# Kernel tuning notes

Hardware: AMD Instinct MI355X
Metric: run time of the kernel (lower is better)

Reference implementation:

```python
import jax, jax.numpy as jnp
import numpy as np

N = 100000   # num nodes
E = 600000   # num edges
H = 128      # hidden dim
R = 8        # num relations
B = 4        # num bases


def setup_inputs() -> dict:
    key = jax.random.key(0)
    ks = jax.random.split(key, 12)
    return {
        "node_ids": jnp.arange(N, dtype=jnp.int64 if jax.config.jax_enable_x64 else jnp.int32),
        "src": jax.random.randint(ks[0], (E,), 0, N),
        "dst": jax.random.randint(ks[1], (E,), 0, N),
        "etype": jax.random.randint(ks[2], (E,), 0, R),
        "embedding": jax.random.normal(ks[3], (N, H), dtype=jnp.float32),
        "V1": jax.random.normal(ks[4], (B, H, H), dtype=jnp.float32) * 0.05,
        "comp1": jax.random.normal(ks[5], (R, B), dtype=jnp.float32),
        "loop1": jax.random.normal(ks[6], (H, H), dtype=jnp.float32) * 0.05,
        "bias1": jax.random.normal(ks[7], (H,), dtype=jnp.float32) * 0.05,
        "V2": jax.random.normal(ks[8], (B, H, H), dtype=jnp.float32) * 0.05,
        "comp2": jax.random.normal(ks[9], (R, B), dtype=jnp.float32),
        "loop2": jax.random.normal(ks[10], (H, H), dtype=jnp.float32) * 0.05,
        "bias2": jax.random.normal(ks[11], (H,), dtype=jnp.float32) * 0.05,
    }


def _rgcn_layer(h, src, dst, etype, V, comp, loopW, bias, activate):
    # basis decomposition: W_r = sum_b comp[r,b] * V[b]   -> [R, in, out]
    W = jnp.einsum('rb,bio->rio', comp, V)
    # transform all nodes under all relations once (avoids per-edge GEMM): [N, R, out]
    hw = jnp.einsum('ni,rio->nro', h, W)
    # gather per-edge message for its (src, relation): [E, out]
    m = hw[src, etype]
    # scatter-sum aggregation at destination nodes
    agg = jax.ops.segment_sum(m, dst, num_segments=h.shape[0])
    out = agg + bias + h @ loopW  # bias + self-loop
    return jax.nn.relu(out) if activate else out


def reference(node_ids, src, dst, etype, embedding,
              V1, comp1, loop1, bias1,
              V2, comp2, loop2, bias2):
    h = embedding[node_ids]                       # EmbeddingLayer
    h = _rgcn_layer(h, src, dst, etype, V1, comp1, loop1, bias1, activate=True)
    h = _rgcn_layer(h, src, dst, etype, V2, comp2, loop2, bias2, activate=False)
    return h
```

## Files before the change

kernel.cpp:

```cpp
#include <hip/hip_runtime.h>
#include <hip/hip_bf16.h>

#define NN 100000
#define NE 600000
#define HH 128
#define NB 4
#define TILE 2048
#define NTILES ((NN + TILE - 1) / TILE)

typedef __attribute__((ext_vector_type(8))) short bf16x8;
typedef __attribute__((ext_vector_type(4))) float f32x4;
typedef __attribute__((ext_vector_type(4))) float vfloat4;
typedef __attribute__((ext_vector_type(4))) unsigned short ushort4v;

static __device__ __forceinline__ short f2bf(float f) {
  unsigned u = __float_as_uint(f);
  unsigned r = (u + 0x7fffu + ((u >> 16) & 1u)) >> 16;
  return (short)r;
}

static __device__ __forceinline__ void build_one(const float* __restrict__ V,
                                                 const float* __restrict__ loopW,
                                                 short* __restrict__ W8, int idx)
{
  int j  = idx & 7;
  int o  = (idx >> 3) & 127;
  int kb = idx >> 10;
  int k  = kb * 8 + j;
  float v;
  if (k < 512) v = V[(size_t)k * HH + o];
  else         v = loopW[(size_t)(k - 512) * HH + o];
  W8[idx] = f2bf(v);
}

__global__ __launch_bounds__(256) void prep_all(
    const float* __restrict__ V1, const float* __restrict__ loop1, short* __restrict__ W81,
    const float* __restrict__ V2, const float* __restrict__ loop2, short* __restrict__ W82,
    const float* __restrict__ emb, short* __restrict__ hbf1)
{
  const int bid = blockIdx.x;
  if (bid < 320) {
    build_one(V1, loop1, W81, bid * 256 + threadIdx.x);
  } else if (bid < 640) {
    build_one(V2, loop2, W82, (bid - 320) * 256 + threadIdx.x);
  } else {
    const int n8 = NN * HH / 8;
    int i = (bid - 640) * 256 + threadIdx.x;
    for (; i < n8; i += 800 * 256) {
      const vfloat4* p = reinterpret_cast<const vfloat4*>(emb + (size_t)i * 8);
      vfloat4 a = p[0], b = p[1];
      bf16x8 o;
#pragma unroll
      for (int j = 0; j < 4; ++j) { o[j] = f2bf(a[j]); o[j + 4] = f2bf(b[j]); }
      reinterpret_cast<bf16x8*>(hbf1)[i] = o;
    }
  }
}


__global__ __launch_bounds__(256) void hist_deg(const int* __restrict__ dst,
                                                int* __restrict__ deg)
{
  int e = blockIdx.x * blockDim.x + threadIdx.x;
  if (e < NE) atomicAdd(&deg[dst[e]], 1);
}

__global__ __launch_bounds__(256) void scan_tiles(const int* __restrict__ deg,
                                                  int* __restrict__ tilesum)
{
  __shared__ int red[256];
  const int tid = threadIdx.x;
  int base = blockIdx.x * TILE + tid * 8;
  int s = 0;
#pragma unroll
  for (int j = 0; j < 8; ++j) {
    int i = base + j;
    if (i < NN) s += deg[i];
  }
  red[tid] = s;
  __syncthreads();
  for (int off = 128; off > 0; off >>= 1) {
    if (tid < off) red[tid] += red[tid + off];
    __syncthreads();
  }
  if (tid == 0) tilesum[blockIdx.x] = red[0];
}

__global__ __launch_bounds__(256) void scan_final(const int* deg,
                                                  const int* __restrict__ tilesum,
                                                  int* __restrict__ rowptr,
                                                  int* cursor)
{
  __shared__ int lds[256];
  const int tid = threadIdx.x;
  int pre = 0;
  for (int t = 0; t < NTILES; ++t)
    if (t < blockIdx.x) pre += tilesum[t];

  int base = blockIdx.x * TILE + tid * 8;
  int d[8];
  int s = 0;
#pragma unroll
  for (int j = 0; j < 8; ++j) {
    int i = base + j;
    d[j] = (i < NN) ? deg[i] : 0;
    s += d[j];
  }
  lds[tid] = s;
  __syncthreads();
  for (int off = 1; off < 256; off <<= 1) {
    int t = (tid >= off) ? lds[tid - off] : 0;
    __syncthreads();
    lds[tid] += t;
    __syncthreads();
  }
  int run = pre + lds[tid] - s;
#pragma unroll
  for (int j = 0; j < 8; ++j) {
    int i = base + j;
    if (i < NN) {
      rowptr[i] = run;
      cursor[i] = run;
      run += d[j];
    }
  }
  if (blockIdx.x == NTILES - 1 && tid == 255)
    rowptr[NN] = pre + lds[255];
}

__global__ __launch_bounds__(256) void scatter_edges(
    const int* __restrict__ src, const int* __restrict__ dst, const int* __restrict__ ety,
    int* __restrict__ cursor, int* __restrict__ csr)
{
  int e = blockIdx.x * blockDim.x + threadIdx.x;
  if (e >= NE) return;
  int d = dst[e];
  int p = atomicAdd(&cursor[d], 1);
  csr[p] = src[e] | (ety[e] << 20);
}

template<int FINAL>
__global__ __launch_bounds__(512, 6) void rgcn_fused(
    const int* __restrict__ rowptr, const int* __restrict__ csr,
    const float* __restrict__ comp,
    const short* __restrict__ hbf,
    const short* __restrict__ W8,
    const float* __restrict__ bias,
    short* __restrict__ outH,
    float* __restrict__ outF)
{
  __shared__ bf16x8 gl[32][64];
  __shared__ bf16x8 wl[2][512];

  const int tid  = threadIdx.x;
  const int wave = tid >> 6;
  const int lane = tid & 63;
  const int b  = lane >> 4;
  const int q  = lane & 15;
  const int base = blockIdx.x * 32;
  const int l4 = lane * 4;

  const int mt = wave >> 2;
  const int ct0 = (wave & 3) * 2;
  const int mynode = base + mt * 16 + q;

  const bf16x8* wsrc = reinterpret_cast<const bf16x8*>(W8);
  bf16x8 w0reg = wsrc[tid];

  const char* hbytes = reinterpret_cast<const char*>(hbf);
  unsigned* glu = reinterpret_cast<unsigned*>(gl);

#pragma unroll 1
  for (int pp = 0; pp < 2; ++pp) {
    const int row0 = wave * 4 + pp * 2;
    const int row1 = row0 + 1;
    int       i0 = __builtin_amdgcn_readfirstlane(rowptr[base + row0]);
    const int E0 = __builtin_amdgcn_readfirstlane(rowptr[base + row0 + 1]);
    int       i1 = E0;
    const int E1 = __builtin_amdgcn_readfirstlane(rowptr[base + row1 + 1]);

    float a0[8] = {0.f, 0.f, 0.f, 0.f, 0.f, 0.f, 0.f, 0.f};
    float a1[8] = {0.f, 0.f, 0.f, 0.f, 0.f, 0.f, 0.f, 0.f};

    while (i0 < E0 || i1 < E1) {
      const bool d0 = i0 < E0, d1 = i1 < E1;
      unsigned hq[8];
      float    cq[8][4];
      if (d0) {
#pragma unroll
        for (int j = 0; j < 4; ++j) {
          const int idx = i0 + j;
          const bool v = idx < E0;
          const int e = __builtin_amdgcn_readfirstlane(csr[v ? idx : E0 - 1]);
          hq[j] = *reinterpret_cast<const unsigned*>(
              hbytes + (((size_t)(e & 0xFFFFF)) << 8) + l4);
#pragma unroll
          for (int B = 0; B < 4; ++B)
            cq[j][B] = v ? comp[(e >> 20) * NB + B] : 0.f;
        }
      }
      if (d1) {
#pragma unroll
        for (int j = 0; j < 4; ++j) {
          const int idx = i1 + j;
          const bool v = idx < E1;
          const int e = __builtin_amdgcn_readfirstlane(csr[v ? idx : E1 - 1]);
          hq[4 + j] = *reinterpret_cast<const unsigned*>(
              hbytes + (((size_t)(e & 0xFFFFF)) << 8) + l4);
#pragma unroll
          for (int B = 0; B < 4; ++B)
            cq[4 + j][B] = v ? comp[(e >> 20) * NB + B] : 0.f;
        }
      }
      if (d0) {
#pragma unroll
        for (int j = 0; j < 4; ++j) {
          const float lo = __uint_as_float(hq[j] << 16);
          const float hi = __uint_as_float(hq[j] & 0xffff0000u);
#pragma unroll
          for (int B = 0; B < 4; ++B) {
            a0[2 * B]     += cq[j][B] * lo;
            a0[2 * B + 1] += cq[j][B] * hi;
          }
        }
        i0 += 4;
      }
      if (d1) {
#pragma unroll
        for (int j = 0; j < 4; ++j) {
          const float lo = __uint_as_float(hq[4 + j] << 16);
          const float hi = __uint_as_float(hq[4 + j] & 0xffff0000u);
#pragma unroll
          for (int B = 0; B < 4; ++B) {
            a1[2 * B]     += cq[4 + j][B] * lo;
            a1[2 * B + 1] += cq[4 + j][B] * hi;
          }
        }
        i1 += 4;
      }
    }

#pragma unroll
    for (int B = 0; B < 4; ++B) {
      unsigned w0 = ((unsigned)(unsigned short)f2bf(a0[2 * B + 1]) << 16) |
                    (unsigned short)f2bf(a0[2 * B]);
      unsigned w1 = ((unsigned)(unsigned short)f2bf(a1[2 * B + 1]) << 16) |
                    (unsigned short)f2bf(a1[2 * B]);
      const int s = B * 16 + (lane >> 2);
      glu[row0 * 256 + ((s ^ (row0 & 7)) << 2) + (lane & 3)] = w0;
      glu[row1 * 256 + ((s ^ (row1 & 7)) << 2) + (lane & 3)] = w1;
    }
  }

  const bf16x8* ha = reinterpret_cast<const bf16x8*>(hbf + (size_t)mynode * HH);
  bf16x8 hreg[4];
#pragma unroll
  for (int j = 0; j < 4; ++j) hreg[j] = ha[j * 4 + b];

  wl[0][tid] = w0reg;
  __syncthreads();

  const int r  = q;
  const int g8 = b;

  f32x4 acc0 = {0.f, 0.f, 0.f, 0.f};
  f32x4 acc1 = {0.f, 0.f, 0.f, 0.f};

#pragma unroll 1
  for (int ks = 0; ks < 20; ++ks) {
    const int cur = ks & 1;
    bf16x8 nxt;
    if (ks < 19) nxt = wsrc[(ks + 1) * 512 + tid];
    bf16x8 a = (ks < 16) ? gl[mt * 16 + r][(ks * 4 + g8) ^ (r & 7)] : hreg[ks - 16];
    bf16x8 w0 = wl[cur][g8 * 128 + (ct0 + 0) * 16 + r];
    bf16x8 w1 = wl[cur][g8 * 128 + (ct0 + 1) * 16 + r];
    acc0 = __builtin_amdgcn_mfma_f32_16x16x32_bf16(w0, a, acc0, 0, 0, 0);
    acc1 = __builtin_amdgcn_mfma_f32_16x16x32_bf16(w1, a, acc1, 0, 0, 0);
    if (ks < 19) wl[cur ^ 1][tid] = nxt;
    __syncthreads();
  }

  if (FINAL) {
    float* glf = reinterpret_cast<float*>(gl);
#pragma unroll
    for (int c = 0; c < 2; ++c) {
      const f32x4 acc = c ? acc1 : acc0;
      const int row = mt * 16 + r;
      const int o = (ct0 + c) * 16 + g8 * 4;
      vfloat4 bs = *reinterpret_cast<const vfloat4*>(bias + o);
      vfloat4 x;
#pragma unroll
      for (int rr = 0; rr < 4; ++rr) x[rr] = acc[rr] + bs[rr];
      const int s = (ct0 + c) * 4 + g8;
      const int phys = s ^ (row & 7);
      *reinterpret_cast<vfloat4*>(glf + row * 128 + phys * 4) = x;
    }
    __syncthreads();
#pragma unroll
    for (int p = 0; p < 2; ++p) {
      const int flat = p * 512 + tid;
      const int row = flat >> 5, s = flat & 31;
      const int phys = s ^ (row & 7);
      vfloat4 x = *reinterpret_cast<const vfloat4*>(glf + row * 128 + phys * 4);
      *reinterpret_cast<vfloat4*>(outF + (size_t)(base + row) * HH + s * 4) = x;
    }
  } else {
    short* glb = reinterpret_cast<short*>(gl);
#pragma unroll
    for (int c = 0; c < 2; ++c) {
      const f32x4 acc = c ? acc1 : acc0;
      const int row = mt * 16 + r;
      const int o = (ct0 + c) * 16 + g8 * 4;
      vfloat4 bs = *reinterpret_cast<const vfloat4*>(bias + o);
      ushort4v sv;
#pragma unroll
      for (int rr = 0; rr < 4; ++rr)
        sv[rr] = (unsigned short)f2bf(fmaxf(acc[rr] + bs[rr], 0.f));
      const int u8 = (ct0 + c) * 4 + g8;
      const int phys16 = (u8 >> 1) ^ (row & 7);
      *reinterpret_cast<ushort4v*>(glb + row * 128 + phys16 * 8 + (u8 & 1) * 4) = sv;
    }
    __syncthreads();
    {
      const int row = tid >> 4, s16 = tid & 15;
      const int phys = s16 ^ (row & 7);
      bf16x8 x = *reinterpret_cast<const bf16x8*>(glb + row * 128 + phys * 8);
      *reinterpret_cast<bf16x8*>(outH + (size_t)(base + row) * HH + s16 * 8) = x;
    }
  }
}

extern "C" void kernel_launch(void* const* d_in, const int* in_sizes, int n_in,
                              void* d_out, int out_size, void* d_ws, size_t ws_size,
                              hipStream_t stream)
{
  const int*   srcp  = (const int*)d_in[1];
  const int*   dstp  = (const int*)d_in[2];
  const int*   etp   = (const int*)d_in[3];
  const float* emb   = (const float*)d_in[4];
  const float* V1    = (const float*)d_in[5];
  const float* comp1 = (const float*)d_in[6];
  const float* loop1 = (const float*)d_in[7];
  const float* bias1 = (const float*)d_in[8];
  const float* V2    = (const float*)d_in[9];
  const float* comp2 = (const float*)d_in[10];
  const float* loop2 = (const float*)d_in[11];
  const float* bias2 = (const float*)d_in[12];
  float* out = (float*)d_out;

  char* ws = (char*)d_ws;
  short* Wt1     = (short*)(ws);
  short* Wt2     = (short*)(ws + 163840);
  short* hbf1    = (short*)(ws + 327680);
  short* hbf2    = (short*)(ws + 25927680);
  int*   deg     = (int*)  (ws + 51527680);
  int*   rowptr  = (int*)  (ws + 51927680);
  int*   csr     = (int*)  (ws + 52327696);
  int*   tilesum = (int*)  (ws + 54727696);

  const int fused_blocks = NN / 32;
  const int e_blocks     = (NE + 255) / 256;

  hipMemsetAsync(deg, 0, NN * sizeof(int), stream);
  hipLaunchKernelGGL(hist_deg, dim3(e_blocks), dim3(256), 0, stream, dstp, deg);
  hipLaunchKernelGGL(scan_tiles, dim3(NTILES), dim3(256), 0, stream, deg, tilesum);
  hipLaunchKernelGGL(scan_final, dim3(NTILES), dim3(256), 0, stream,
                     deg, tilesum, rowptr, deg);
  hipLaunchKernelGGL(scatter_edges, dim3(e_blocks), dim3(256), 0, stream,
                     srcp, dstp, etp, deg, csr);

  hipLaunchKernelGGL(prep_all, dim3(1440), dim3(256), 0, stream,
                     V1, loop1, Wt1, V2, loop2, Wt2, emb, hbf1);

  hipLaunchKernelGGL((rgcn_fused<0>), dim3(fused_blocks), dim3(512), 0, stream,
                     rowptr, csr, comp1, hbf1, Wt1, bias1, hbf2, (float*)nullptr);

  hipLaunchKernelGGL((rgcn_fused<1>), dim3(fused_blocks), dim3(512), 0, stream,
                     rowptr, csr, comp2, hbf2, Wt2, bias2, (short*)nullptr, out);
}
```

Measured before the change: 307.1 us.

## Fold degree histogram into prep kernel and gather four rows per wave concurrently

The degree-histogram atomics are merged into the prep_all launch, so weight conversion, embedding conversion and the histogram run as one grid and one kernel launch disappears. The fused RGCN gather loop now walks four destination rows per wave at once instead of two rows in two passes, issuing up to 16 independent edge loads per iteration to hide gather latency. Comp coefficients are now loaded after the gathers rather than alongside them. The extra in-flight loads and four accumulator sets raise register pressure, which may lower occupancy.

```diff
diff --git a/kernel.cpp b/kernel.cpp
--- a/kernel.cpp
+++ b/kernel.cpp
@@ -36,16 +36,20 @@
 __global__ __launch_bounds__(256) void prep_all(
     const float* __restrict__ V1, const float* __restrict__ loop1, short* __restrict__ W81,
     const float* __restrict__ V2, const float* __restrict__ loop2, short* __restrict__ W82,
-    const float* __restrict__ emb, short* __restrict__ hbf1)
+    const float* __restrict__ emb, short* __restrict__ hbf1,
+    const int* __restrict__ dst, int* __restrict__ deg)
 {
   const int bid = blockIdx.x;
   if (bid < 320) {
     build_one(V1, loop1, W81, bid * 256 + threadIdx.x);
   } else if (bid < 640) {
     build_one(V2, loop2, W82, (bid - 320) * 256 + threadIdx.x);
+  } else if (bid < 2984) {
+    int e = (bid - 640) * 256 + threadIdx.x;
+    if (e < NE) atomicAdd(&deg[dst[e]], 1);
   } else {
     const int n8 = NN * HH / 8;
-    int i = (bid - 640) * 256 + threadIdx.x;
+    int i = (bid - 2984) * 256 + threadIdx.x;
     for (; i < n8; i += 800 * 256) {
       const vfloat4* p = reinterpret_cast<const vfloat4*>(emb + (size_t)i * 8);
       vfloat4 a = p[0], b = p[1];
@@ -57,13 +61,6 @@
   }
 }
 
-
-__global__ __launch_bounds__(256) void hist_deg(const int* __restrict__ dst,
-                                                int* __restrict__ deg)
-{
-  int e = blockIdx.x * blockDim.x + threadIdx.x;
-  if (e < NE) atomicAdd(&deg[dst[e]], 1);
-}
 
 __global__ __launch_bounds__(256) void scan_tiles(const int* __restrict__ deg,
                                                   int* __restrict__ tilesum)
@@ -170,85 +167,69 @@
   const char* hbytes = reinterpret_cast<const char*>(hbf);
   unsigned* glu = reinterpret_cast<unsigned*>(gl);
 
-#pragma unroll 1
-  for (int pp = 0; pp < 2; ++pp) {
-    const int row0 = wave * 4 + pp * 2;
-    const int row1 = row0 + 1;
-    int       i0 = __builtin_amdgcn_readfirstlane(rowptr[base + row0]);
-    const int E0 = __builtin_amdgcn_readfirstlane(rowptr[base + row0 + 1]);
-    int       i1 = E0;
-    const int E1 = __builtin_amdgcn_readfirstlane(rowptr[base + row1 + 1]);
-
-    float a0[8] = {0.f, 0.f, 0.f, 0.f, 0.f, 0.f, 0.f, 0.f};
-    float a1[8] = {0.f, 0.f, 0.f, 0.f, 0.f, 0.f, 0.f, 0.f};
-
-    while (i0 < E0 || i1 < E1) {
-      const bool d0 = i0 < E0, d1 = i1 < E1;
-      unsigned hq[8];
-      float    cq[8][4];
-      if (d0) {
-#pragma unroll
-        for (int j = 0; j < 4; ++j) {
-          const int idx = i0 + j;
-          const bool v = idx < E0;
-          const int e = __builtin_amdgcn_readfirstlane(csr[v ? idx : E0 - 1]);
-          hq[j] = *reinterpret_cast<const unsigned*>(
-              hbytes + (((size_t)(e & 0xFFFFF)) << 8) + l4);
-#pragma unroll
-          for (int B = 0; B < 4; ++B)
-            cq[j][B] = v ? comp[(e >> 20) * NB + B] : 0.f;
+  {
+    const int r0 = wave * 4;
+    int ii[4], EE[4];
+    ii[0] = __builtin_amdgcn_readfirstlane(rowptr[base + r0]);
+    EE[0] = __builtin_amdgcn_readfirstlane(rowptr[base + r0 + 1]);
+    ii[1] = EE[0];
+    EE[1] = __builtin_amdgcn_readfirstlane(rowptr[base + r0 + 2]);
+    ii[2] = EE[1];
+    EE[2] = __builtin_amdgcn_readfirstlane(rowptr[base + r0 + 3]);
+    ii[3] = EE[2];
+    EE[3] = __builtin_amdgcn_readfirstlane(rowptr[base + r0 + 4]);
+
+    float acc[4][8] = {};
+
+    while (ii[0] < EE[0] || ii[1] < EE[1] || ii[2] < EE[2] || ii[3] < EE[3]) {
+      unsigned hq[16];
+      int es[16];
+#pragma unroll
+      for (int n = 0; n < 4; ++n) {
+        if (ii[n] < EE[n]) {
+#pragma unroll
+          for (int j = 0; j < 4; ++j) {
+            const int idx = ii[n] + j;
+            const int e = __builtin_amdgcn_readfirstlane(
+                csr[idx < EE[n] ? idx : EE[n] - 1]);
+            es[n * 4 + j] = e;
+            hq[n * 4 + j] = *reinterpret_cast<const unsigned*>(
+                hbytes + (((size_t)(e & 0xFFFFF)) << 8) + l4);
+          }
         }
       }
-      if (d1) {
-#pragma unroll
-        for (int j = 0; j < 4; ++j) {
-          const int idx = i1 + j;
-          const bool v = idx < E1;
-          const int e = __builtin_amdgcn_readfirstlane(csr[v ? idx : E1 - 1]);
-          hq[4 + j] = *reinterpret_cast<const unsigned*>(
-              hbytes + (((size_t)(e & 0xFFFFF)) << 8) + l4);
-#pragma unroll
-          for (int B = 0; B < 4; ++B)
-            cq[4 + j][B] = v ? comp[(e >> 20) * NB + B] : 0.f;
+#pragma unroll
+      for (int n = 0; n < 4; ++n) {
+        if (ii[n] < EE[n]) {
+#pragma unroll
+          for (int j = 0; j < 4; ++j) {
+            const int idx = ii[n] + j;
+            const bool v = idx < EE[n];
+            const int e = es[n * 4 + j];
+            const float lo = __uint_as_float(hq[n * 4 + j] << 16);
+            const float hi = __uint_as_float(hq[n * 4 + j] & 0xffff0000u);
+#pragma unroll
+            for (int B = 0; B < 4; ++B) {
+              const float c = v ? comp[(e >> 20) * NB + B] : 0.f;
+              acc[n][2 * B]     += c * lo;
+              acc[n][2 * B + 1] += c * hi;
+            }
+          }
+          ii[n] += 4;
         }
       }
-      if (d0) {
-#pragma unroll
-        for (int j = 0; j < 4; ++j) {
-          const float lo = __uint_as_float(hq[j] << 16);
-          const float hi = __uint_as_float(hq[j] & 0xffff0000u);
-#pragma unroll
-          for (int B = 0; B < 4; ++B) {
-            a0[2 * B]     += cq[j][B] * lo;
-            a0[2 * B + 1] += cq[j][B] * hi;
-          }
-        }
-        i0 += 4;
+    }
+
+#pragma unroll
+    for (int n = 0; n < 4; ++n) {
+      const int row = r0 + n;
+#pragma unroll
+      for (int B = 0; B < 4; ++B) {
+        unsigned w = ((unsigned)(unsigned short)f2bf(acc[n][2 * B + 1]) << 16) |
+                     (unsigned short)f2bf(acc[n][2 * B]);
+        const int s = B * 16 + (lane >> 2);
+        glu[row * 256 + ((s ^ (row & 7)) << 2) + (lane & 3)] = w;
       }
-      if (d1) {
-#pragma unroll
-        for (int j = 0; j < 4; ++j) {
-          const float lo = __uint_as_float(hq[4 + j] << 16);
-          const float hi = __uint_as_float(hq[4 + j] & 0xffff0000u);
-#pragma unroll
-          for (int B = 0; B < 4; ++B) {
-            a1[2 * B]     += cq[4 + j][B] * lo;
-            a1[2 * B + 1] += cq[4 + j][B] * hi;
-          }
-        }
-        i1 += 4;
-      }
-    }
-
-#pragma unroll
-    for (int B = 0; B < 4; ++B) {
-      unsigned w0 = ((unsigned)(unsigned short)f2bf(a0[2 * B + 1]) << 16) |
-                    (unsigned short)f2bf(a0[2 * B]);
-      unsigned w1 = ((unsigned)(unsigned short)f2bf(a1[2 * B + 1]) << 16) |
-                    (unsigned short)f2bf(a1[2 * B]);
-      const int s = B * 16 + (lane >> 2);
-      glu[row0 * 256 + ((s ^ (row0 & 7)) << 2) + (lane & 3)] = w0;
-      glu[row1 * 256 + ((s ^ (row1 & 7)) << 2) + (lane & 3)] = w1;
     }
   }
 
@@ -362,16 +343,16 @@
   const int e_blocks     = (NE + 255) / 256;
 
   hipMemsetAsync(deg, 0, NN * sizeof(int), stream);
-  hipLaunchKernelGGL(hist_deg, dim3(e_blocks), dim3(256), 0, stream, dstp, deg);
+
+  hipLaunchKernelGGL(prep_all, dim3(3784), dim3(256), 0, stream,
+                     V1, loop1, Wt1, V2, loop2, Wt2, emb, hbf1, dstp, deg);
+
   hipLaunchKernelGGL(scan_tiles, dim3(NTILES), dim3(256), 0, stream, deg, tilesum);
   hipLaunchKernelGGL(scan_final, dim3(NTILES), dim3(256), 0, stream,
                      deg, tilesum, rowptr, deg);
   hipLaunchKernelGGL(scatter_edges, dim3(e_blocks), dim3(256), 0, stream,
                      srcp, dstp, etp, deg, csr);
 
-  hipLaunchKernelGGL(prep_all, dim3(1440), dim3(256), 0, stream,
-                     V1, loop1, Wt1, V2, loop2, Wt2, emb, hbf1);
-
   hipLaunchKernelGGL((rgcn_fused<0>), dim3(fused_blocks), dim3(512), 0, stream,
                      rowptr, csr, comp1, hbf1, Wt1, bias1, hbf2, (float*)nullptr);
 
```

Measured after the change: 289.1 us, median of 2. 5.9% less time.
